# Optimization experiments

Measured on AMD Instinct MI355X. Metric: run time of the kernel, lower is better.

The kernel has to match this reference:

```python
import jax, jax.numpy as jnp
import numpy as np

IMAGE_SIZE = 256
NEAR, FAR, EPS = 0.1, 100.0, 0.001
BACKGROUND = (0.0, 0.0, 0.0)
B, F, TS = 1, 256, 4


def setup_inputs() -> dict:
    key = jax.random.key(0)
    k1, k2, k3, k4, k5 = jax.random.split(key, 5)
    # small random triangles in NDC with depth in (near, far)
    center = jax.random.uniform(k1, (B, F, 1, 2), minval=-1.0, maxval=1.0)
    offs = jax.random.uniform(k2, (B, F, 3, 2), minval=-0.15, maxval=0.15)
    xy = center + offs                                   # [B,F,3,2]
    zc = jax.random.uniform(k3, (B, F, 1, 1), minval=1.0, maxval=10.0)
    zo = jax.random.uniform(k4, (B, F, 3, 1), minval=-0.05, maxval=0.05)
    faces = jnp.concatenate([xy, zc + zo], axis=-1).astype(jnp.float32)  # [B,F,3,3]
    textures = jax.random.uniform(k5, (B, F, TS, TS, TS, 3), dtype=jnp.float32)
    return {"faces": faces, "textures": textures}


def _render_one(faces_b, tex_b):
    """faces_b: [F,3,3], tex_b: [F,TS,TS,TS,3] -> image [3,H,W]."""
    S = IMAGE_SIZE
    P = S * S
    x, y, z = faces_b[..., 0], faces_b[..., 1], faces_b[..., 2]  # each [F,3]

    # pixel centers in NDC; row 0 is top of image (y = +1 side)
    coo = (2.0 * jnp.arange(S, dtype=jnp.float32) + 1.0 - S) / S
    Y, X = jnp.meshgrid(-coo, coo, indexing="ij")
    px = X.reshape(-1)  # [P]
    py = Y.reshape(-1)

    # barycentric coordinates for every (pixel, face) pair -> [P,F]
    denom = (y[:, 1] - y[:, 2]) * (x[:, 0] - x[:, 2]) + (x[:, 2] - x[:, 1]) * (y[:, 0] - y[:, 2])  # [F]
    denom = jnp.where(jnp.abs(denom) < 1e-12, 1e-12, denom)
    dx2 = px[:, None] - x[None, :, 2]
    dy2 = py[:, None] - y[None, :, 2]
    w0 = ((y[:, 1] - y[:, 2])[None] * dx2 + (x[:, 2] - x[:, 1])[None] * dy2) / denom[None]
    w1 = ((y[:, 2] - y[:, 0])[None] * dx2 + (x[:, 0] - x[:, 2])[None] * dy2) / denom[None]
    w2 = 1.0 - w0 - w1
    inside = (w0 >= 0.0) & (w1 >= 0.0) & (w2 >= 0.0)

    # clipped / renormalized weights (as in the CUDA kernel)
    c0 = jnp.clip(w0, 0.0, 1.0)
    c1 = jnp.clip(w1, 0.0, 1.0)
    c2 = jnp.clip(w2, 0.0, 1.0)
    ssum = jnp.maximum(c0 + c1 + c2, 1e-12)
    c0, c1, c2 = c0 / ssum, c1 / ssum, c2 / ssum

    # perspective-correct interpolated depth
    inv_z = c0 / z[None, :, 0] + c1 / z[None, :, 1] + c2 / z[None, :, 2]
    zp = 1.0 / jnp.maximum(jnp.abs(inv_z), 1e-12) * jnp.sign(inv_z + 1e-30)
    valid = inside & (zp > NEAR) & (zp < FAR)

    # z-buffer: nearest valid face per pixel
    zbuf = jnp.where(valid, zp, jnp.inf)
    fidx = jnp.argmin(zbuf, axis=1)                      # [P]
    ar = jnp.arange(P)
    hit = jnp.isfinite(zbuf[ar, fidx])                   # [P]

    # gather winner quantities
    wc = jnp.stack([c0[ar, fidx], c1[ar, fidx], c2[ar, fidx]], axis=1)  # [P,3]
    zw = z[fidx]                                         # [P,3] vertex depths
    zpw = zp[ar, fidx]                                   # [P]

    # trilinear 3D texture sampling (8-corner blend, as in forward_texture_sampling)
    tif = wc * (TS - 1) * (zpw[:, None] / zw)            # [P,3]
    tif = jnp.clip(tif, 0.0, TS - 1 - EPS)
    ti0 = jnp.floor(tif).astype(jnp.int32)
    frac = tif - ti0.astype(jnp.float32)
    wtex = tex_b[fidx]                                   # [P,TS,TS,TS,3]
    pixel = jnp.zeros((P, 3), dtype=faces_b.dtype)
    for corner in range(8):
        bits = [(corner >> k) & 1 for k in range(3)]
        w = jnp.ones((P,), dtype=faces_b.dtype)
        idx = []
        for k, bit in enumerate(bits):
            w = w * (frac[:, k] if bit else 1.0 - frac[:, k])
            idx.append(jnp.minimum(ti0[:, k] + bit, TS - 1))
        pixel = pixel + w[:, None] * wtex[ar, idx[0], idx[1], idx[2]]  # [P,3]

    bg = jnp.asarray(BACKGROUND, dtype=faces_b.dtype)
    pixel = jnp.where(hit[:, None], pixel, bg[None, :])
    return pixel.reshape(S, S, 3).transpose(2, 0, 1)      # [3,H,W]


def reference(faces, textures):
    return jax.vmap(_render_one)(faces, textures)        # [B,3,H,W]
```

## Files before the change

kernel.cpp:

```cpp
#include <hip/hip_runtime.h>
#include <math.h>

#define IMG_S 256
#define FCAP 512

#define FADD(a,b) __fadd_rn((a),(b))
#define FSUB(a,b) __fsub_rn((a),(b))
#define FMUL(a,b) __fmul_rn((a),(b))
#define FDIV(a,b) __fdiv_rn((a),(b))

__global__ __launch_bounds__(256) void raster_kernel(
    const float* __restrict__ faces,
    const float* __restrict__ tex,
    float* __restrict__ out,
    int F)
{
    __shared__ float4 s_A[FCAP], s_B[FCAP], s_C[FCAP];
    __shared__ int    s_cnt[4];

    const int tid  = threadIdx.x;
    const int lane = tid & 63;
    const int wid  = tid >> 6;

    const int tile_x = blockIdx.x & 15;
    const int tile_y = blockIdx.x >> 4;
    const int col0 = tile_x * 16;
    const int row0 = tile_y * 16;

    const float px_min = (float)(2*col0        + 1 - IMG_S) / (float)IMG_S;
    const float px_max = (float)(2*(col0+15)   + 1 - IMG_S) / (float)IMG_S;
    const float py_max = -(float)(2*row0       + 1 - IMG_S) / (float)IMG_S;
    const float py_min = -(float)(2*(row0+15)  + 1 - IMG_S) / (float)IMG_S;
    const float MARGIN = 1e-3f;

    int nk = 0;
    for (int f0 = 0; f0 < F; f0 += 256) {
        const int f = f0 + tid;
        bool keep = false;
        float x0=0,y0=0,z0=0,x1=0,y1=0,z1=0,x2=0,y2=0,z2=0,den=0.f;
        if (f < F) {
            const float* fp = faces + (size_t)f * 9;
            x0=fp[0]; y0=fp[1]; z0=fp[2];
            x1=fp[3]; y1=fp[4]; z1=fp[5];
            x2=fp[6]; y2=fp[7]; z2=fp[8];
            den = FADD(FMUL(FSUB(y1,y2), FSUB(x0,x2)),
                       FMUL(FSUB(x2,x1), FSUB(y0,y2)));
            float bxmin = fminf(fminf(x0,x1),x2), bxmax = fmaxf(fmaxf(x0,x1),x2);
            float bymin = fminf(fminf(y0,y1),y2), bymax = fmaxf(fmaxf(y0,y1),y2);
            keep = (bxmin - MARGIN <= px_max) && (bxmax + MARGIN >= px_min)
                && (bymin - MARGIN <= py_max) && (bymax + MARGIN >= py_min);
            keep = keep || (fabsf(den) < 1e-9f);
        }
        unsigned long long m = __ballot(keep);
        if (lane == 0) s_cnt[wid] = (int)__popcll(m);
        __syncthreads();
        int base = nk;
        #pragma unroll
        for (int w = 0; w < 4; ++w) if (w < wid) base += s_cnt[w];
        if (keep) {
            int pos = base + (int)__popcll(m & ((1ull << lane) - 1ull));
            if (pos < FCAP) {
                float dn = den;
                if (fabsf(dn) < 1e-12f) dn = 1e-12f;
                s_A[pos] = make_float4(FSUB(y1,y2), FSUB(x2,x1), FSUB(y2,y0), FSUB(x0,x2));
                s_B[pos] = make_float4(x2, y2, dn, z0);
                s_C[pos] = make_float4(z1, z2, __int_as_float(f), 0.0f);
            }
        }
        nk += s_cnt[0] + s_cnt[1] + s_cnt[2] + s_cnt[3];
        __syncthreads();
    }
    if (nk > FCAP) nk = FCAP;

    const int col = col0 + (tid & 15);
    const int row = row0 + (tid >> 4);
    const float px = (float)(2*col + 1 - IMG_S) / (float)IMG_S;
    const float py = -(float)(2*row + 1 - IMG_S) / (float)IMG_S;

    float bestz = INFINITY;
    int   besti = -1;
    float bc0=0.f, bc1=0.f, bc2=0.f, bzp=0.f;

    for (int i = 0; i < nk; ++i) {
        const float4 va = s_A[i];
        const float4 vb = s_B[i];
        const float dx2 = FSUB(px, vb.x);
        const float dy2 = FSUB(py, vb.y);
        const float num0 = FADD(FMUL(va.x,dx2), FMUL(va.y,dy2));
        const float num1 = FADD(FMUL(va.z,dx2), FMUL(va.w,dy2));
        const float dn = vb.z;
        const bool dpos = dn > 0.0f;
        const bool in0 = (num0 == 0.0f) | ((num0 > 0.0f) == dpos);
        const bool in1 = (num1 == 0.0f) | ((num1 > 0.0f) == dpos);
        if (!(in0 && in1)) continue;

        const float w0 = FDIV(num0, dn);
        const float w1 = FDIV(num1, dn);
        const float w2 = FSUB(FSUB(1.0f, w0), w1);
        if (!(w2 >= 0.0f)) continue;

        float cc0 = fminf(fmaxf(w0, 0.0f), 1.0f);
        float cc1 = fminf(fmaxf(w1, 0.0f), 1.0f);
        float cc2 = fminf(fmaxf(w2, 0.0f), 1.0f);
        const float ss = fmaxf(FADD(FADD(cc0,cc1),cc2), 1e-12f);
        cc0 = FDIV(cc0, ss); cc1 = FDIV(cc1, ss); cc2 = FDIV(cc2, ss);

        const float4 vc = s_C[i];
        const float iz = FADD(FADD(FDIV(cc0, vb.w), FDIV(cc1, vc.x)), FDIV(cc2, vc.y));
        const float t  = FADD(iz, 1e-30f);
        const float sg = (t > 0.0f) ? 1.0f : ((t < 0.0f) ? -1.0f : 0.0f);
        const float zp = FMUL(FDIV(1.0f, fmaxf(fabsf(iz), 1e-12f)), sg);

        if (zp > 0.1f && zp < 100.0f && zp < bestz) {
            bestz = zp; besti = i;
            bc0 = cc0; bc1 = cc1; bc2 = cc2; bzp = zp;
        }
    }

    float pr = 0.0f, pg = 0.0f, pb = 0.0f;
    if (besti >= 0) {
        const int i = besti;
        const float4 vb = s_B[i];
        const float4 vc = s_C[i];
        const float zs[3] = { vb.w, vc.x, vc.y };
        const float wc[3] = { bc0, bc1, bc2 };
        int   ti0[3];
        float fr[3];
        #pragma unroll
        for (int k = 0; k < 3; ++k) {
            float v = FMUL(FMUL(wc[k], 3.0f), FDIV(bzp, zs[k]));
            v = fminf(fmaxf(v, 0.0f), 2.999f);
            float fl = floorf(v);
            ti0[k] = (int)fl;
            fr[k]  = FSUB(v, fl);
        }
        const float* tp = tex + (size_t)__float_as_int(vc.z) * 192;
        #pragma unroll
        for (int corner = 0; corner < 8; ++corner) {
            float w = 1.0f;
            int idx[3];
            #pragma unroll
            for (int k = 0; k < 3; ++k) {
                int bit = (corner >> k) & 1;
                w = FMUL(w, bit ? fr[k] : FSUB(1.0f, fr[k]));
                int id = ti0[k] + bit; if (id > 3) id = 3;
                idx[k] = id;
            }
            const float* tv = tp + (size_t)(((idx[0]*4 + idx[1])*4 + idx[2])*3);
            pr = FADD(pr, FMUL(w, tv[0]));
            pg = FADD(pg, FMUL(w, tv[1]));
            pb = FADD(pb, FMUL(w, tv[2]));
        }
    }

    const int p = row * IMG_S + col;
    out[p]                 = pr;
    out[IMG_S*IMG_S + p]   = pg;
    out[2*IMG_S*IMG_S + p] = pb;
}

extern "C" void kernel_launch(void* const* d_in, const int* in_sizes, int n_in,
                              void* d_out, int out_size, void* d_ws, size_t ws_size,
                              hipStream_t stream) {
    const float* faces = (const float*)d_in[0];
    const float* tex   = (const float*)d_in[1];
    float* out = (float*)d_out;
    const int F = in_sizes[0] / 9;

    const int grid = (IMG_S / 16) * (IMG_S / 16);
    raster_kernel<<<grid, 256, 0, stream>>>(faces, tex, out, F);
}
```

Measured before the change: 10.92 us.

## Use 8x8 tiles with four threads per pixel splitting faces and texture corners

Tiles shrink from 16x16 to 8x8, so the grid grows to 1024 blocks and each tile's culled face list gets shorter. Each pixel is now handled by four lanes that stride over the face list, then combine their nearest hits with xor shuffles, breaking depth ties by lowest index. The same four lanes each take two of the eight trilinear texture corners and sum the results with shuffles. The cost is four times as many face-list builds, extra shuffle traffic, and a smaller FCAP of 256 that could truncate the list if many faces overlap one tile. The texture sum order also changes, so float rounding may differ slightly from before.

New measurement: 10.19 us. 1.07x faster.

```diff
diff --git a/kernel.cpp b/kernel.cpp
--- a/kernel.cpp
+++ b/kernel.cpp
@@ -1,8 +1,9 @@
 #include <hip/hip_runtime.h>
 #include <math.h>
+#include <limits.h>
 
 #define IMG_S 256
-#define FCAP 512
+#define FCAP 256
 
 #define FADD(a,b) __fadd_rn((a),(b))
 #define FSUB(a,b) __fsub_rn((a),(b))
@@ -22,15 +23,15 @@
     const int lane = tid & 63;
     const int wid  = tid >> 6;
 
-    const int tile_x = blockIdx.x & 15;
-    const int tile_y = blockIdx.x >> 4;
-    const int col0 = tile_x * 16;
-    const int row0 = tile_y * 16;
+    const int tile_x = blockIdx.x & 31;
+    const int tile_y = blockIdx.x >> 5;
+    const int col0 = tile_x * 8;
+    const int row0 = tile_y * 8;
 
-    const float px_min = (float)(2*col0        + 1 - IMG_S) / (float)IMG_S;
-    const float px_max = (float)(2*(col0+15)   + 1 - IMG_S) / (float)IMG_S;
-    const float py_max = -(float)(2*row0       + 1 - IMG_S) / (float)IMG_S;
-    const float py_min = -(float)(2*(row0+15)  + 1 - IMG_S) / (float)IMG_S;
+    const float px_min = (float)(2*col0       + 1 - IMG_S) / (float)IMG_S;
+    const float px_max = (float)(2*(col0+7)   + 1 - IMG_S) / (float)IMG_S;
+    const float py_max = -(float)(2*row0      + 1 - IMG_S) / (float)IMG_S;
+    const float py_min = -(float)(2*(row0+7)  + 1 - IMG_S) / (float)IMG_S;
     const float MARGIN = 1e-3f;
 
     int nk = 0;
@@ -72,16 +73,18 @@
     }
     if (nk > FCAP) nk = FCAP;
 
-    const int col = col0 + (tid & 15);
-    const int row = row0 + (tid >> 4);
+    const int slot = lane & 3;
+    const int pidx = wid * 16 + (lane >> 2);
+    const int col = col0 + (pidx & 7);
+    const int row = row0 + (pidx >> 3);
     const float px = (float)(2*col + 1 - IMG_S) / (float)IMG_S;
     const float py = -(float)(2*row + 1 - IMG_S) / (float)IMG_S;
 
     float bestz = INFINITY;
-    int   besti = -1;
-    float bc0=0.f, bc1=0.f, bc2=0.f, bzp=0.f;
+    int   key   = INT_MAX;
+    float bc0=0.f, bc1=0.f, bc2=0.f;
 
-    for (int i = 0; i < nk; ++i) {
+    for (int i = slot; i < nk; i += 4) {
         const float4 va = s_A[i];
         const float4 vb = s_B[i];
         const float dx2 = FSUB(px, vb.x);
@@ -112,23 +115,34 @@
         const float zp = FMUL(FDIV(1.0f, fmaxf(fabsf(iz), 1e-12f)), sg);
 
         if (zp > 0.1f && zp < 100.0f && zp < bestz) {
-            bestz = zp; besti = i;
-            bc0 = cc0; bc1 = cc1; bc2 = cc2; bzp = zp;
+            bestz = zp; key = i;
+            bc0 = cc0; bc1 = cc1; bc2 = cc2;
         }
     }
 
+    #pragma unroll
+    for (int d = 1; d <= 2; d <<= 1) {
+        const float oz = __shfl_xor(bestz, d);
+        const int   ok = __shfl_xor(key, d);
+        const float o0 = __shfl_xor(bc0, d);
+        const float o1 = __shfl_xor(bc1, d);
+        const float o2 = __shfl_xor(bc2, d);
+        const bool take = (oz < bestz) || ((oz == bestz) && (ok < key));
+        if (take) { bestz = oz; key = ok; bc0 = o0; bc1 = o1; bc2 = o2; }
+    }
+
     float pr = 0.0f, pg = 0.0f, pb = 0.0f;
-    if (besti >= 0) {
-        const int i = besti;
-        const float4 vb = s_B[i];
-        const float4 vc = s_C[i];
+    const bool hit = (key != INT_MAX);
+    if (hit) {
+        const float4 vb = s_B[key];
+        const float4 vc = s_C[key];
         const float zs[3] = { vb.w, vc.x, vc.y };
         const float wc[3] = { bc0, bc1, bc2 };
         int   ti0[3];
         float fr[3];
         #pragma unroll
         for (int k = 0; k < 3; ++k) {
-            float v = FMUL(FMUL(wc[k], 3.0f), FDIV(bzp, zs[k]));
+            float v = FMUL(FMUL(wc[k], 3.0f), FDIV(bestz, zs[k]));
             v = fminf(fmaxf(v, 0.0f), 2.999f);
             float fl = floorf(v);
             ti0[k] = (int)fl;
@@ -136,7 +150,8 @@
         }
         const float* tp = tex + (size_t)__float_as_int(vc.z) * 192;
         #pragma unroll
-        for (int corner = 0; corner < 8; ++corner) {
+        for (int c = 0; c < 2; ++c) {
+            const int corner = slot * 2 + c;
             float w = 1.0f;
             int idx[3];
             #pragma unroll
@@ -151,12 +166,20 @@
             pg = FADD(pg, FMUL(w, tv[1]));
             pb = FADD(pb, FMUL(w, tv[2]));
         }
+        #pragma unroll
+        for (int d = 1; d <= 2; d <<= 1) {
+            pr = FADD(pr, __shfl_xor(pr, d));
+            pg = FADD(pg, __shfl_xor(pg, d));
+            pb = FADD(pb, __shfl_xor(pb, d));
+        }
     }
 
-    const int p = row * IMG_S + col;
-    out[p]                 = pr;
-    out[IMG_S*IMG_S + p]   = pg;
-    out[2*IMG_S*IMG_S + p] = pb;
+    if (slot == 0) {
+        const int p = row * IMG_S + col;
+        out[p]                 = pr;
+        out[IMG_S*IMG_S + p]   = pg;
+        out[2*IMG_S*IMG_S + p] = pb;
+    }
 }
 
 extern "C" void kernel_launch(void* const* d_in, const int* in_sizes, int n_in,
@@ -167,6 +190,6 @@
     float* out = (float*)d_out;
     const int F = in_sizes[0] / 9;
 
-    const int grid = (IMG_S / 16) * (IMG_S / 16);
+    const int grid = (IMG_S / 8) * (IMG_S / 8);
     raster_kernel<<<grid, 256, 0, stream>>>(faces, tex, out, F);
 }
```
